# Kernel tuning notes

Measured on AMD Instinct MI355X. Metric: run time of the kernel, lower is better.

## Reference

```python
import jax, jax.numpy as jnp
import numpy as np

B, T, D, H = 2, 2048, 1024, 16
DK = D // H


def setup_inputs() -> dict:
    key = jax.random.key(0)
    ks = jax.random.split(key, 5)
    scale = 1.0 / np.sqrt(D)  # keep activations sane (xavier-like)
    return {
        "x": jax.random.normal(ks[0], (B, T, D), dtype=jnp.float32),
        "mask": jnp.zeros((B, 1, 1, T), dtype=jnp.float32),
        "Wq": jax.random.normal(ks[1], (D, D), dtype=jnp.float32) * scale,
        "Wk": jax.random.normal(ks[2], (D, D), dtype=jnp.float32) * scale,
        "Wv": jax.random.normal(ks[3], (D, D), dtype=jnp.float32) * scale,
        "Wo": jax.random.normal(ks[4], (D, D), dtype=jnp.float32) * scale,
    }


def reference(x, mask, Wq, Wk, Wv, Wo):
    b, t, d = x.shape
    h = H
    dk = d // h
    inv_sqrt_dk = jnp.asarray(1.0 / np.sqrt(dk), dtype=x.dtype)
    q = (x @ Wq).reshape(b, t, h, dk) * inv_sqrt_dk  # [b,t,h,dk]
    k = (x @ Wk).reshape(b, t, h, dk)
    v = (x @ Wv).reshape(b, t, h, dk)
    scores = jnp.einsum('bthd,blhd->bhtl', q, k) + mask  # [b,h,t,l]
    A = jax.nn.softmax(scores, axis=-1)
    # NOTE: faithful to the source: values are indexed by t (query pos), not l.
    o = jnp.einsum('bhtl,bthd->bhtd', A, v)  # [b,h,t,dk]
    # Faithful to source's raw reshape of (b,h,t,dk) -> (b,T,d)
    o = o.reshape(b, t, d)
    # nn.Linear without bias: y = o @ Wo^T
    return o @ Wo.T
```

## Files before the change

### kernel.cpp

```cpp
#include <hip/hip_runtime.h>
#include <hip/hip_bf16.h>


using bf16 = __hip_bfloat16;
typedef __attribute__((ext_vector_type(8))) short bf16x8;
typedef __attribute__((ext_vector_type(4))) float f32x4;

__device__ __forceinline__ void gld_lds16(const void* g, void* l) {
    __builtin_amdgcn_global_load_lds(
        (const __attribute__((address_space(1))) void*)g,
        (__attribute__((address_space(3))) void*)l, 16, 0, 0);
}

__global__ __launch_bounds__(256) void prep(const float* __restrict__ x,
                                            const float* __restrict__ Wv,
                                            const float* __restrict__ Wo,
                                            bf16* __restrict__ xb,
                                            bf16* __restrict__ WvT,
                                            bf16* __restrict__ Wob) {
    __shared__ float tile[64][65];
    const int id = blockIdx.x;
    const int t  = threadIdx.x;
    if (id < 256) {
        const int bx = id & 15, by = id >> 4;
        const int c = t & 63, r4 = t >> 6;
#pragma unroll
        for (int p = 0; p < 16; ++p) {
            int r = p * 4 + r4;
            tile[r][c] = Wv[(size_t)(by * 64 + r) * 1024 + bx * 64 + c];
        }
        __syncthreads();
#pragma unroll
        for (int p = 0; p < 16; ++p) {
            int r = p * 4 + r4;
            WvT[(size_t)(bx * 64 + r) * 1024 + by * 64 + c] = __float2bfloat16(tile[c][r]);
        }
    } else if (id < 4352) {
        const int i = (id - 256) * 256 + t;
        const float4 v = ((const float4*)x)[i];
        bf16 o[4] = {__float2bfloat16(v.x), __float2bfloat16(v.y),
                     __float2bfloat16(v.z), __float2bfloat16(v.w)};
        ((ulong1*)xb)[i] = *(ulong1*)o;
    } else {
        const int i = (id - 4352) * 256 + t;
        const float4 v = ((const float4*)Wo)[i];
        bf16 o[4] = {__float2bfloat16(v.x), __float2bfloat16(v.y),
                     __float2bfloat16(v.z), __float2bfloat16(v.w)};
        ((ulong1*)Wob)[i] = *(ulong1*)o;
    }
}

__device__ __forceinline__ void storeC(float v, bf16* p)  { *p = __float2bfloat16(v); }
__device__ __forceinline__ void storeC(float v, float* p) { *p = v; }

template <bool PERMUTE, typename OutT>
__global__ __launch_bounds__(256) void gemm_bt(const bf16* __restrict__ A,
                                               const bf16* __restrict__ Bt,
                                               OutT* __restrict__ C) {
    __shared__ __align__(16) bf16 st[3][6144];

    const int tid  = threadIdx.x;
    const int wave = tid >> 6;
    const int lane = tid & 63;
    const int m0 = blockIdx.x * 128;
    const int n0 = blockIdx.y * 64;

    const int wr = (wave >> 1) * 64;
    const int wc = (wave & 1) * 32;

    const int srow = tid >> 2;
    const int scol = (((tid & 3) ^ ((tid >> 3) & 3)) & 3) * 8;
    const bf16* gA = A  + (size_t)(m0 + srow) * 1024 + scol;
    const bf16* gB = Bt + (size_t)(n0 + srow) * 1024 + scol;
    const int woff = wave * 512;

    f32x4 acc[4][2];
#pragma unroll
    for (int i = 0; i < 4; ++i)
#pragma unroll
        for (int j = 0; j < 2; ++j)
            acc[i][j] = (f32x4){0.f, 0.f, 0.f, 0.f};

    const int fr = lane & 15;
    const int q8 = ((((lane >> 4) ^ (lane >> 1)) & 3)) * 8;

#pragma unroll
    for (int b = 0; b < 2; ++b) {
        bf16* s = st[b];
        const int kt = b * 32;
        gld_lds16(gA + kt,             s + woff);
        gld_lds16(gA + kt + 64 * 1024, s + 2048 + woff);
        gld_lds16(gB + kt,             s + 4096 + woff);
    }

#pragma unroll 1
    for (int i = 0; i < 32; ++i) {
        if (i < 31)
            asm volatile("s_waitcnt vmcnt(3)" ::: "memory");
        else
            asm volatile("s_waitcnt vmcnt(0)" ::: "memory");
        asm volatile("s_barrier" ::: "memory");
        if (i < 30) {
            const int kt = (i + 2) * 32;
            bf16* s = st[(i + 2) % 3];
            gld_lds16(gA + kt,             s + woff);
            gld_lds16(gA + kt + 64 * 1024, s + 2048 + woff);
            gld_lds16(gB + kt,             s + 4096 + woff);
        }

        const bf16* sAb = st[i % 3];
        const bf16* sBb = st[i % 3] + 4096;
        bf16x8 aF[4], bF[2];
#pragma unroll
        for (int ii = 0; ii < 4; ++ii)
            aF[ii] = *(const bf16x8*)&sAb[(wr + ii * 16 + fr) * 32 + q8];
#pragma unroll
        for (int j = 0; j < 2; ++j)
            bF[j] = *(const bf16x8*)&sBb[(wc + j * 16 + fr) * 32 + q8];
#pragma unroll
        for (int ii = 0; ii < 4; ++ii)
#pragma unroll
            for (int j = 0; j < 2; ++j)
                acc[ii][j] = __builtin_amdgcn_mfma_f32_16x16x32_bf16(
                    aF[ii], bF[j], acc[ii][j], 0, 0, 0);
    }

#pragma unroll
    for (int i = 0; i < 4; ++i) {
#pragma unroll
        for (int j = 0; j < 2; ++j) {
            const int col = n0 + wc + j * 16 + (lane & 15);
#pragma unroll
            for (int r = 0; r < 4; ++r) {
                const int row = m0 + wr + i * 16 + (lane >> 4) * 4 + r;
                if (PERMUTE) {
                    const int b = row >> 11, t = row & 2047;
                    const int h = col >> 6,  k = col & 63;
                    const int rr = (b << 11) | (h << 7) | (t >> 4);
                    const int cc = ((t & 15) << 6) | k;
                    storeC(acc[i][j][r], &C[(size_t)rr * 1024 + cc]);
                } else {
                    storeC(acc[i][j][r], &C[(size_t)row * 1024 + col]);
                }
            }
        }
    }
}

extern "C" void kernel_launch(void* const* d_in, const int* in_sizes, int n_in,
                              void* d_out, int out_size, void* d_ws, size_t ws_size,
                              hipStream_t stream) {
    (void)in_sizes; (void)n_in; (void)out_size; (void)ws_size;
    const float* x  = (const float*)d_in[0];
    const float* Wv = (const float*)d_in[4];
    const float* Wo = (const float*)d_in[5];
    float* out = (float*)d_out;

    bf16* xb    = (bf16*)d_ws;
    bf16* WvT   = xb    + 4096 * 1024;
    bf16* Wob   = WvT   + 1024 * 1024;
    bf16* vperm = Wob   + 1024 * 1024;

    prep<<<5376, 256, 0, stream>>>(x, Wv, Wo, xb, WvT, Wob);
    gemm_bt<true,  bf16 ><<<dim3(32, 16), 256, 0, stream>>>(xb, WvT, vperm);
    gemm_bt<false, float><<<dim3(32, 16), 256, 0, stream>>>(vperm, Wob, out);
}
```

Before: 114.4 us.

## Fuse fp32-to-bf16 conversion of x and Wo into GEMM tile loads

The GEMMs now stage fp32 tiles of x and Wo directly into LDS with an XOR swizzle and convert them to bf16 in registers before the MFMAs. This drops the separate conversion pass and the bf16 copies held in the workspace, so prep only transposes Wv. In exchange each GEMM reads twice the bytes for the fp32 operand, uses more LDS per block, and adds conversion work to the inner loop. Launch bounds now request two blocks per SIMD.

```diff
diff --git a/kernel.cpp b/kernel.cpp
--- a/kernel.cpp
+++ b/kernel.cpp
@@ -12,52 +12,46 @@
         (__attribute__((address_space(3))) void*)l, 16, 0, 0);
 }
 
-__global__ __launch_bounds__(256) void prep(const float* __restrict__ x,
-                                            const float* __restrict__ Wv,
-                                            const float* __restrict__ Wo,
-                                            bf16* __restrict__ xb,
-                                            bf16* __restrict__ WvT,
-                                            bf16* __restrict__ Wob) {
+__device__ __forceinline__ bf16x8 cvt8(f32x4 lo, f32x4 hi) {
+    bf16 o[8] = {__float2bfloat16(lo[0]), __float2bfloat16(lo[1]),
+                 __float2bfloat16(lo[2]), __float2bfloat16(lo[3]),
+                 __float2bfloat16(hi[0]), __float2bfloat16(hi[1]),
+                 __float2bfloat16(hi[2]), __float2bfloat16(hi[3])};
+    return *(bf16x8*)o;
+}
+
+__global__ __launch_bounds__(256) void prep(const float* __restrict__ Wv,
+                                            bf16* __restrict__ WvT) {
     __shared__ float tile[64][65];
     const int id = blockIdx.x;
     const int t  = threadIdx.x;
-    if (id < 256) {
-        const int bx = id & 15, by = id >> 4;
-        const int c = t & 63, r4 = t >> 6;
-#pragma unroll
-        for (int p = 0; p < 16; ++p) {
-            int r = p * 4 + r4;
-            tile[r][c] = Wv[(size_t)(by * 64 + r) * 1024 + bx * 64 + c];
-        }
-        __syncthreads();
-#pragma unroll
-        for (int p = 0; p < 16; ++p) {
-            int r = p * 4 + r4;
-            WvT[(size_t)(bx * 64 + r) * 1024 + by * 64 + c] = __float2bfloat16(tile[c][r]);
-        }
-    } else if (id < 4352) {
-        const int i = (id - 256) * 256 + t;
-        const float4 v = ((const float4*)x)[i];
-        bf16 o[4] = {__float2bfloat16(v.x), __float2bfloat16(v.y),
-                     __float2bfloat16(v.z), __float2bfloat16(v.w)};
-        ((ulong1*)xb)[i] = *(ulong1*)o;
-    } else {
-        const int i = (id - 4352) * 256 + t;
-        const float4 v = ((const float4*)Wo)[i];
-        bf16 o[4] = {__float2bfloat16(v.x), __float2bfloat16(v.y),
-                     __float2bfloat16(v.z), __float2bfloat16(v.w)};
-        ((ulong1*)Wob)[i] = *(ulong1*)o;
+    const int bx = id & 15, by = id >> 4;
+    const int c = t & 63, r4 = t >> 6;
+#pragma unroll
+    for (int p = 0; p < 16; ++p) {
+        int r = p * 4 + r4;
+        tile[r][c] = Wv[(size_t)(by * 64 + r) * 1024 + bx * 64 + c];
+    }
+    __syncthreads();
+#pragma unroll
+    for (int p = 0; p < 16; ++p) {
+        int r = p * 4 + r4;
+        WvT[(size_t)(bx * 64 + r) * 1024 + by * 64 + c] = __float2bfloat16(tile[c][r]);
     }
 }
 
 __device__ __forceinline__ void storeC(float v, bf16* p)  { *p = __float2bfloat16(v); }
 __device__ __forceinline__ void storeC(float v, float* p) { *p = v; }
 
-template <bool PERMUTE, typename OutT>
-__global__ __launch_bounds__(256) void gemm_bt(const bf16* __restrict__ A,
-                                               const bf16* __restrict__ Bt,
-                                               OutT* __restrict__ C) {
-    __shared__ __align__(16) bf16 st[3][6144];
+template <bool PERMUTE, bool AF32, bool BF32, typename OutT>
+__global__ __launch_bounds__(256, 2) void gemm_bt(const void* __restrict__ Av,
+                                                  const void* __restrict__ Bv,
+                                                  OutT* __restrict__ C) {
+    constexpr int ABYTES = AF32 ? 16384 : 8192;
+    constexpr int BBYTES = BF32 ? 8192  : 4096;
+    constexpr int BUFB   = ABYTES + BBYTES;
+    constexpr int NDMA   = (AF32 ? 4 : 2) + (BF32 ? 2 : 1);
+    __shared__ __align__(16) char st[3 * BUFB];
 
     const int tid  = threadIdx.x;
     const int wave = tid >> 6;
@@ -68,11 +62,46 @@
     const int wr = (wave >> 1) * 64;
     const int wc = (wave & 1) * 32;
 
-    const int srow = tid >> 2;
-    const int scol = (((tid & 3) ^ ((tid >> 3) & 3)) & 3) * 8;
-    const bf16* gA = A  + (size_t)(m0 + srow) * 1024 + scol;
-    const bf16* gB = Bt + (size_t)(n0 + srow) * 1024 + scol;
-    const int woff = wave * 512;
+    const float* gA32 = nullptr; const bf16* gAb = nullptr;
+    if constexpr (AF32)
+        gA32 = (const float*)Av + (size_t)(m0 + (tid >> 3)) * 1024
+             + (((tid & 7) ^ ((tid >> 3) & 7)) * 4);
+    else
+        gAb  = (const bf16*)Av + (size_t)(m0 + (tid >> 2)) * 1024
+             + (((tid & 3) ^ ((tid >> 3) & 3)) * 8);
+    const float* gB32 = nullptr; const bf16* gBb = nullptr;
+    if constexpr (BF32)
+        gB32 = (const float*)Bv + (size_t)(n0 + (tid >> 3)) * 1024
+             + (((tid & 7) ^ ((tid >> 3) & 7)) * 4);
+    else
+        gBb  = (const bf16*)Bv + (size_t)(n0 + (tid >> 2)) * 1024
+             + (((tid & 3) ^ ((tid >> 3) & 3)) * 8);
+
+    const int wb = wave * 1024;
+
+    auto stage = [&](int kt, int buf) {
+        char* base = st + buf * BUFB;
+        if constexpr (AF32) {
+            const float* s = gA32 + kt * 32;
+            gld_lds16(s,             base + wb);
+            gld_lds16(s + 32 * 1024, base + 4096  + wb);
+            gld_lds16(s + 64 * 1024, base + 8192  + wb);
+            gld_lds16(s + 96 * 1024, base + 12288 + wb);
+        } else {
+            const bf16* s = gAb + kt * 32;
+            gld_lds16(s,             base + wb);
+            gld_lds16(s + 64 * 1024, base + 4096 + wb);
+        }
+        char* bb = base + ABYTES;
+        if constexpr (BF32) {
+            const float* s = gB32 + kt * 32;
+            gld_lds16(s,             bb + wb);
+            gld_lds16(s + 32 * 1024, bb + 4096 + wb);
+        } else {
+            const bf16* s = gBb + kt * 32;
+            gld_lds16(s, bb + wb);
+        }
+    };
 
     f32x4 acc[4][2];
 #pragma unroll
@@ -82,41 +111,58 @@
             acc[i][j] = (f32x4){0.f, 0.f, 0.f, 0.f};
 
     const int fr = lane & 15;
-    const int q8 = ((((lane >> 4) ^ (lane >> 1)) & 3)) * 8;
-
-#pragma unroll
-    for (int b = 0; b < 2; ++b) {
-        bf16* s = st[b];
-        const int kt = b * 32;
-        gld_lds16(gA + kt,             s + woff);
-        gld_lds16(gA + kt + 64 * 1024, s + 2048 + woff);
-        gld_lds16(gB + kt,             s + 4096 + woff);
-    }
+    const int q8  = (((lane >> 4) ^ (lane >> 1)) & 3) * 8;
+    const int s32 = (((lane >> 4) * 2) ^ (lane & 7)) * 4;
+
+    stage(0, 0);
+    stage(1, 1);
 
 #pragma unroll 1
     for (int i = 0; i < 32; ++i) {
-        if (i < 31)
-            asm volatile("s_waitcnt vmcnt(3)" ::: "memory");
-        else
+        if (i < 31) {
+            if constexpr (NDMA == 5)
+                asm volatile("s_waitcnt vmcnt(5)" ::: "memory");
+            else
+                asm volatile("s_waitcnt vmcnt(4)" ::: "memory");
+        } else {
             asm volatile("s_waitcnt vmcnt(0)" ::: "memory");
+        }
         asm volatile("s_barrier" ::: "memory");
-        if (i < 30) {
-            const int kt = (i + 2) * 32;
-            bf16* s = st[(i + 2) % 3];
-            gld_lds16(gA + kt,             s + woff);
-            gld_lds16(gA + kt + 64 * 1024, s + 2048 + woff);
-            gld_lds16(gB + kt,             s + 4096 + woff);
-        }
-
-        const bf16* sAb = st[i % 3];
-        const bf16* sBb = st[i % 3] + 4096;
+        if (i < 30)
+            stage(i + 2, (i + 2) % 3);
+
+        const char* buf = st + (i % 3) * BUFB;
         bf16x8 aF[4], bF[2];
-#pragma unroll
-        for (int ii = 0; ii < 4; ++ii)
-            aF[ii] = *(const bf16x8*)&sAb[(wr + ii * 16 + fr) * 32 + q8];
-#pragma unroll
-        for (int j = 0; j < 2; ++j)
-            bF[j] = *(const bf16x8*)&sBb[(wc + j * 16 + fr) * 32 + q8];
+        if constexpr (AF32) {
+            const float* sA = (const float*)buf;
+#pragma unroll
+            for (int ii = 0; ii < 4; ++ii) {
+                const int rb = (wr + ii * 16 + fr) * 32;
+                f32x4 lo = *(const f32x4*)&sA[rb + s32];
+                f32x4 hi = *(const f32x4*)&sA[rb + (s32 ^ 4)];
+                aF[ii] = cvt8(lo, hi);
+            }
+        } else {
+            const bf16* sA = (const bf16*)buf;
+#pragma unroll
+            for (int ii = 0; ii < 4; ++ii)
+                aF[ii] = *(const bf16x8*)&sA[(wr + ii * 16 + fr) * 32 + q8];
+        }
+        if constexpr (BF32) {
+            const float* sB = (const float*)(buf + ABYTES);
+#pragma unroll
+            for (int j = 0; j < 2; ++j) {
+                const int rb = (wc + j * 16 + fr) * 32;
+                f32x4 lo = *(const f32x4*)&sB[rb + s32];
+                f32x4 hi = *(const f32x4*)&sB[rb + (s32 ^ 4)];
+                bF[j] = cvt8(lo, hi);
+            }
+        } else {
+            const bf16* sB = (const bf16*)(buf + ABYTES);
+#pragma unroll
+            for (int j = 0; j < 2; ++j)
+                bF[j] = *(const bf16x8*)&sB[(wc + j * 16 + fr) * 32 + q8];
+        }
 #pragma unroll
         for (int ii = 0; ii < 4; ++ii)
 #pragma unroll
@@ -156,12 +202,10 @@
     const float* Wo = (const float*)d_in[5];
     float* out = (float*)d_out;
 
-    bf16* xb    = (bf16*)d_ws;
-    bf16* WvT   = xb    + 4096 * 1024;
-    bf16* Wob   = WvT   + 1024 * 1024;
-    bf16* vperm = Wob   + 1024 * 1024;
-
-    prep<<<5376, 256, 0, stream>>>(x, Wv, Wo, xb, WvT, Wob);
-    gemm_bt<true,  bf16 ><<<dim3(32, 16), 256, 0, stream>>>(xb, WvT, vperm);
-    gemm_bt<false, float><<<dim3(32, 16), 256, 0, stream>>>(vperm, Wob, out);
-}
+    bf16* WvT   = (bf16*)d_ws;
+    bf16* vperm = WvT + 1024 * 1024;
+
+    prep<<<256, 256, 0, stream>>>(Wv, WvT);
+    gemm_bt<true,  true,  false, bf16 ><<<dim3(32, 16), 256, 0, stream>>>(x, WvT, vperm);
+    gemm_bt<false, false, true,  float><<<dim3(32, 16), 256, 0, stream>>>(vperm, Wo, out);
+}
```

Result: slower. 119.9 us (+4.9%).

## Fuse fp32-to-bf16 conversion of x into the first GEMM's load pipeline

Applied to the files above, without the earlier changes.

Drops the separate x conversion pass from the prep kernel. The first GEMM now loads fp32 x straight into registers, converts it to bf16 and writes it to LDS inside a software pipeline, while B still goes through direct global-to-LDS loads. This removes a full write and re-read of the bf16 copy of x. In exchange it reads twice the A bytes per GEMM block (16 column blocks each reread x in fp32), uses more registers, and needs more involved waitcnt bookkeeping.

```diff
diff --git a/kernel.cpp b/kernel.cpp
--- a/kernel.cpp
+++ b/kernel.cpp
@@ -12,10 +12,16 @@
         (__attribute__((address_space(3))) void*)l, 16, 0, 0);
 }
 
-__global__ __launch_bounds__(256) void prep(const float* __restrict__ x,
-                                            const float* __restrict__ Wv,
+__device__ __forceinline__ bf16x8 cvt8(f32x4 lo, f32x4 hi) {
+    bf16 o[8] = {__float2bfloat16(lo[0]), __float2bfloat16(lo[1]),
+                 __float2bfloat16(lo[2]), __float2bfloat16(lo[3]),
+                 __float2bfloat16(hi[0]), __float2bfloat16(hi[1]),
+                 __float2bfloat16(hi[2]), __float2bfloat16(hi[3])};
+    return *(bf16x8*)o;
+}
+
+__global__ __launch_bounds__(256) void prep(const float* __restrict__ Wv,
                                             const float* __restrict__ Wo,
-                                            bf16* __restrict__ xb,
                                             bf16* __restrict__ WvT,
                                             bf16* __restrict__ Wob) {
     __shared__ float tile[64][65];
@@ -35,14 +41,8 @@
             int r = p * 4 + r4;
             WvT[(size_t)(bx * 64 + r) * 1024 + by * 64 + c] = __float2bfloat16(tile[c][r]);
         }
-    } else if (id < 4352) {
+    } else {
         const int i = (id - 256) * 256 + t;
-        const float4 v = ((const float4*)x)[i];
-        bf16 o[4] = {__float2bfloat16(v.x), __float2bfloat16(v.y),
-                     __float2bfloat16(v.z), __float2bfloat16(v.w)};
-        ((ulong1*)xb)[i] = *(ulong1*)o;
-    } else {
-        const int i = (id - 4352) * 256 + t;
         const float4 v = ((const float4*)Wo)[i];
         bf16 o[4] = {__float2bfloat16(v.x), __float2bfloat16(v.y),
                      __float2bfloat16(v.z), __float2bfloat16(v.w)};
@@ -52,6 +52,139 @@
 
 __device__ __forceinline__ void storeC(float v, bf16* p)  { *p = __float2bfloat16(v); }
 __device__ __forceinline__ void storeC(float v, float* p) { *p = v; }
+
+template <bool PERMUTE, typename OutT>
+__global__ __launch_bounds__(256) void gemm_xa(const float* __restrict__ A32,
+                                               const bf16* __restrict__ Bt,
+                                               OutT* __restrict__ C) {
+    __shared__ __align__(16) bf16 st[3][6144];
+
+    const int tid  = threadIdx.x;
+    const int wave = tid >> 6;
+    const int lane = tid & 63;
+    const int m0 = blockIdx.x * 128;
+    const int n0 = blockIdx.y * 64;
+
+    const int wr = (wave >> 1) * 64;
+    const int wc = (wave & 1) * 32;
+
+    const int cg = (((tid & 3) ^ ((tid >> 3) & 3)) & 3) * 8;
+    const float* gx = A32 + (size_t)(m0 + (tid >> 2)) * 1024 + cg;
+    const int la = (tid >> 2) * 64 + (tid & 3) * 16;
+
+    const bf16* gB = Bt + (size_t)(n0 + (tid >> 2)) * 1024
+                   + ((((tid & 3) ^ ((tid >> 3) & 3)) & 3) * 8);
+    const int woff = wave * 512;
+
+    f32x4 rA[2][4];
+    f32x4 acc[4][2];
+#pragma unroll
+    for (int i = 0; i < 4; ++i)
+#pragma unroll
+        for (int j = 0; j < 2; ++j)
+            acc[i][j] = (f32x4){0.f, 0.f, 0.f, 0.f};
+
+    const int fr = lane & 15;
+    const int q8 = (((lane >> 4) ^ (lane >> 1)) & 3) * 8;
+
+    {
+        const float* p0 = gx;
+        rA[0][0] = *(const f32x4*)p0;
+        rA[0][1] = *(const f32x4*)(p0 + 4);
+        rA[0][2] = *(const f32x4*)(p0 + 65536);
+        rA[0][3] = *(const f32x4*)(p0 + 65536 + 4);
+        const float* p1 = gx + 32;
+        rA[1][0] = *(const f32x4*)p1;
+        rA[1][1] = *(const f32x4*)(p1 + 4);
+        rA[1][2] = *(const f32x4*)(p1 + 65536);
+        rA[1][3] = *(const f32x4*)(p1 + 65536 + 4);
+        char* d0 = (char*)st[0];
+        *(bf16x8*)(d0 + la)        = cvt8(rA[0][0], rA[0][1]);
+        *(bf16x8*)(d0 + la + 4096) = cvt8(rA[0][2], rA[0][3]);
+        char* d1 = (char*)st[1];
+        *(bf16x8*)(d1 + la)        = cvt8(rA[1][0], rA[1][1]);
+        *(bf16x8*)(d1 + la + 4096) = cvt8(rA[1][2], rA[1][3]);
+        asm volatile("" ::: "memory");
+        const float* p2 = gx + 64;
+        rA[0][0] = *(const f32x4*)p2;
+        rA[0][1] = *(const f32x4*)(p2 + 4);
+        rA[0][2] = *(const f32x4*)(p2 + 65536);
+        rA[0][3] = *(const f32x4*)(p2 + 65536 + 4);
+        gld_lds16(gB, st[0] + 4096 + woff);
+        asm volatile("" ::: "memory");
+        const float* p3 = gx + 96;
+        rA[1][0] = *(const f32x4*)p3;
+        rA[1][1] = *(const f32x4*)(p3 + 4);
+        rA[1][2] = *(const f32x4*)(p3 + 65536);
+        rA[1][3] = *(const f32x4*)(p3 + 65536 + 4);
+        gld_lds16(gB + 32, st[1] + 4096 + woff);
+    }
+
+#pragma unroll 2
+    for (int i = 0; i < 32; ++i) {
+        if (i <= 28)
+            asm volatile("s_waitcnt vmcnt(5)" ::: "memory");
+        else if (i <= 30)
+            asm volatile("s_waitcnt vmcnt(1)" ::: "memory");
+        else
+            asm volatile("s_waitcnt vmcnt(0)" ::: "memory");
+        asm volatile("s_waitcnt lgkmcnt(0)" ::: "memory");
+        asm volatile("s_barrier" ::: "memory");
+
+        f32x4 (&rW)[4] = rA[i & 1];
+        if (i <= 29) {
+            char* dA = (char*)st[(i + 2) % 3];
+            *(bf16x8*)(dA + la)        = cvt8(rW[0], rW[1]);
+            *(bf16x8*)(dA + la + 4096) = cvt8(rW[2], rW[3]);
+        }
+        if (i <= 27) {
+            const float* p = gx + (i + 4) * 32;
+            rW[0] = *(const f32x4*)p;
+            rW[1] = *(const f32x4*)(p + 4);
+            rW[2] = *(const f32x4*)(p + 65536);
+            rW[3] = *(const f32x4*)(p + 65536 + 4);
+        }
+        if (i <= 29)
+            gld_lds16(gB + (i + 2) * 32, st[(i + 2) % 3] + 4096 + woff);
+
+        const bf16* sAb = st[i % 3];
+        const bf16* sBb = st[i % 3] + 4096;
+        bf16x8 aF[4], bF[2];
+#pragma unroll
+        for (int ii = 0; ii < 4; ++ii)
+            aF[ii] = *(const bf16x8*)&sAb[(wr + ii * 16 + fr) * 32 + q8];
+#pragma unroll
+        for (int j = 0; j < 2; ++j)
+            bF[j] = *(const bf16x8*)&sBb[(wc + j * 16 + fr) * 32 + q8];
+#pragma unroll
+        for (int ii = 0; ii < 4; ++ii)
+#pragma unroll
+            for (int j = 0; j < 2; ++j)
+                acc[ii][j] = __builtin_amdgcn_mfma_f32_16x16x32_bf16(
+                    aF[ii], bF[j], acc[ii][j], 0, 0, 0);
+    }
+
+#pragma unroll
+    for (int i = 0; i < 4; ++i) {
+#pragma unroll
+        for (int j = 0; j < 2; ++j) {
+            const int col = n0 + wc + j * 16 + (lane & 15);
+#pragma unroll
+            for (int r = 0; r < 4; ++r) {
+                const int row = m0 + wr + i * 16 + (lane >> 4) * 4 + r;
+                if (PERMUTE) {
+                    const int b = row >> 11, t = row & 2047;
+                    const int h = col >> 6,  k = col & 63;
+                    const int rr = (b << 11) | (h << 7) | (t >> 4);
+                    const int cc = ((t & 15) << 6) | k;
+                    storeC(acc[i][j][r], &C[(size_t)rr * 1024 + cc]);
+                } else {
+                    storeC(acc[i][j][r], &C[(size_t)row * 1024 + col]);
+                }
+            }
+        }
+    }
+}
 
 template <bool PERMUTE, typename OutT>
 __global__ __launch_bounds__(256) void gemm_bt(const bf16* __restrict__ A,
@@ -156,12 +289,11 @@
     const float* Wo = (const float*)d_in[5];
     float* out = (float*)d_out;
 
-    bf16* xb    = (bf16*)d_ws;
-    bf16* WvT   = xb    + 4096 * 1024;
-    bf16* Wob   = WvT   + 1024 * 1024;
-    bf16* vperm = Wob   + 1024 * 1024;
-
-    prep<<<5376, 256, 0, stream>>>(x, Wv, Wo, xb, WvT, Wob);
-    gemm_bt<true,  bf16 ><<<dim3(32, 16), 256, 0, stream>>>(xb, WvT, vperm);
+    bf16* WvT   = (bf16*)d_ws;
+    bf16* Wob   = WvT + 1024 * 1024;
+    bf16* vperm = Wob + 1024 * 1024;
+
+    prep<<<1280, 256, 0, stream>>>(Wv, Wo, WvT, Wob);
+    gemm_xa<true,  bf16 ><<<dim3(32, 16), 256, 0, stream>>>(x, WvT, vperm);
     gemm_bt<false, float><<<dim3(32, 16), 256, 0, stream>>>(vperm, Wob, out);
 }
```

After: 115.4 us. About the same (+0.9%).
